# Kernel optimization log

Hardware: AMD Instinct MI355X
Metric: run time of the kernel (lower is better)

The kernel has to match this reference:

```python
import jax, jax.numpy as jnp
import numpy as np

B, S, D, H = 2, 2048, 512, 8
DK = D // H
MASK_VALUE = -1e9


def setup_inputs() -> dict:
    key = jax.random.key(0)
    ks = jax.random.split(key, 12)
    scale = 1.0 / np.sqrt(D)
    inp = {
        "query": jax.random.normal(ks[0], (B, S, D), jnp.float32),
        "key": jax.random.normal(ks[1], (B, S, D), jnp.float32),
        "value": jax.random.normal(ks[2], (B, S, D), jnp.float32),
        # causal mask, broadcastable over batch and heads
        "mask": jnp.tril(jnp.ones((S, S), jnp.int32))[None, None, :, :],
        "Wq": jax.random.normal(ks[3], (D, D), jnp.float32) * scale,
        "bq": jax.random.normal(ks[4], (D,), jnp.float32) * scale,
        "Wk": jax.random.normal(ks[5], (D, D), jnp.float32) * scale,
        "bk": jax.random.normal(ks[6], (D,), jnp.float32) * scale,
        "Wv": jax.random.normal(ks[7], (D, D), jnp.float32) * scale,
        "bv": jax.random.normal(ks[8], (D,), jnp.float32) * scale,
        "Wo": jax.random.normal(ks[9], (D, D), jnp.float32) * scale,
        "bo": jax.random.normal(ks[10], (D,), jnp.float32) * scale,
    }
    return inp


def reference(query, key, value, mask, Wq, bq, Wk, bk, Wv, bv, Wo, bo):
    # linear projections (torch Linear: x @ W.T + b)
    q = query @ Wq.T + bq
    k = key @ Wk.T + bk
    v = value @ Wv.T + bv
    # split heads: [B,S,D] -> [B,H,S,DK]
    q = q.reshape(B, S, H, DK).transpose(0, 2, 1, 3)
    k = k.reshape(B, S, H, DK).transpose(0, 2, 1, 3)
    v = v.reshape(B, S, H, DK).transpose(0, 2, 1, 3)
    # scaled dot-product attention with explicit [B,H,S,S] score matrix
    scores = jnp.einsum("bhqd,bhkd->bhqk", q, k) / jnp.sqrt(jnp.float32(DK))
    scores = jnp.where(mask == 0, jnp.float32(MASK_VALUE), scores)
    attn = jax.nn.softmax(scores, axis=-1)
    x = jnp.einsum("bhqk,bhkd->bhqd", attn, v)
    # merge heads: [B,H,S,DK] -> [B,S,D]
    x = x.transpose(0, 2, 1, 3).reshape(B, S, D)
    return x @ Wo.T + bo
```

## Files before the change

### kernel.cpp

```cpp
#include <hip/hip_runtime.h>
#include <hip/hip_bf16.h>

#define B_   2
#define S_   2048
#define D_   512
#define H_   8
#define DK_  64
#define M_   (B_*S_)

typedef float  floatx4 __attribute__((ext_vector_type(4)));
typedef __bf16 bf16x8  __attribute__((ext_vector_type(8)));

#define MFMA16x16x32(a,b,c) __builtin_amdgcn_mfma_f32_16x16x32_bf16((a),(b),(c),0,0,0)

#define PST 40
#define PBUF 2560

static __device__ __forceinline__ void load_lds16(const void* g, void* l) {
  __builtin_amdgcn_global_load_lds(
      (const __attribute__((address_space(1))) void*)g,
      (__attribute__((address_space(3))) void*)l,
      16, 0, 0);
}

static __device__ __forceinline__ bf16x8 cvt8(float4 a, float4 b) {
  bf16x8 r;
  r[0]=(__bf16)a.x; r[1]=(__bf16)a.y; r[2]=(__bf16)a.z; r[3]=(__bf16)a.w;
  r[4]=(__bf16)b.x; r[5]=(__bf16)b.y; r[6]=(__bf16)b.z; r[7]=(__bf16)b.w;
  return r;
}

static __device__ __forceinline__ int part_idx(int bh, int t, int s) {
  const int g = t >> 3;
  const int basec = (g == 2) ? 16 : ((g == 3) ? 40 : 0);
  return bh*72 + basec + (t - 8*g)*(g + 1) + s;
}


__global__ __launch_bounds__(256) void proj_qkv(
    const float* __restrict__ q_in, const float* __restrict__ k_in,
    const float* __restrict__ v_in,
    const float* __restrict__ Wq32, const float* __restrict__ Wk32,
    const float* __restrict__ Wv32,
    const float* __restrict__ bq, const float* __restrict__ bk,
    const float* __restrict__ bv,
    __bf16* __restrict__ Qb, __bf16* __restrict__ Kb, __bf16* __restrict__ Vtb)
{
  __shared__ __align__(16) __bf16 smem[4*PBUF];

  const int z = blockIdx.z;
  const float* X    = (z==0) ? q_in : (z==1) ? k_in : v_in;
  const float* W32  = (z==0) ? Wq32 : (z==1) ? Wk32 : Wv32;
  const float* bias = (z==0) ? bq : (z==1) ? bk : bv;

  const int m0 = blockIdx.x * 64;
  const int n0 = blockIdx.y * 64;
  const int tid  = threadIdx.x;
  const int w    = tid >> 6;
  const int lane = tid & 63;
  const int lcol = lane & 15;
  const int quad = lane >> 4;

  const int arow = tid >> 2, ac = (tid & 3) * 8;

  floatx4 zero = {0.f,0.f,0.f,0.f};
  floatx4 acc[4] = {zero, zero, zero, zero};

  float4 a0,a1,b0,b1;
  auto ldAB = [&](int k0) {
    const float* pa = X   + (size_t)(m0 + arow)*D_ + k0 + ac;
    const float* pb = W32 + (size_t)(n0 + arow)*D_ + k0 + ac;
    a0 = *(const float4*)pa; a1 = *(const float4*)(pa + 4);
    b0 = *(const float4*)pb; b1 = *(const float4*)(pb + 4);
  };
  auto wrAB = [&](int bsel) {
    *(bf16x8*)(smem + bsel*PBUF + arow*PST + ac)         = cvt8(a0, a1);
    *(bf16x8*)(smem + 2*PBUF + bsel*PBUF + arow*PST + ac) = cvt8(b0, b1);
  };

  ldAB(0); wrAB(0);
  for (int it = 0; it < 16; ++it) {
    __syncthreads();
    const bool havenext = (it + 1 < 16);
    if (havenext) ldAB((it+1)*32);
    const __bf16* ab = smem + (it&1)*PBUF;
    const __bf16* bb = smem + 2*PBUF + (it&1)*PBUF;
    const bf16x8 af = *(const bf16x8*)(ab + (w*16 + lcol)*PST + quad*8);
    bf16x8 bf[4];
#pragma unroll
    for (int nt = 0; nt < 4; ++nt)
      bf[nt] = *(const bf16x8*)(bb + (nt*16 + lcol)*PST + quad*8);
#pragma unroll
    for (int nt = 0; nt < 4; ++nt)
      acc[nt] = MFMA16x16x32(af, bf[nt], acc[nt]);
    if (havenext) wrAB((it+1)&1);
  }

  __syncthreads();
#pragma unroll
  for (int nt = 0; nt < 4; ++nt) {
    const int dk = nt*16 + lcol;
    const float bias_n = bias[n0 + dk];
#pragma unroll
    for (int r = 0; r < 4; ++r) {
      const int klo = w*16 + quad*4 + r;
      const float val = acc[nt][r] + bias_n;
      int off;
      if (z == 0) {
        off = klo*64 + dk;
      } else if (z == 1) {
        off = (((klo>>4)*2 + (dk>>5))*64 + ((dk>>3)&3)*16 + (klo&15))*8 + (dk&7);
      } else {
        off = (((dk>>4)*2 + (klo>>5))*64 + ((klo>>3)&3)*16 + (dk&15))*8 + (klo&7);
      }
      smem[off] = (__bf16)val;
    }
  }
  __syncthreads();

  __bf16* dst = (z==0) ? Qb : (z==1) ? Kb : Vtb;
  const int bb2 = m0 >> 11;
  const int hh  = n0 >> 6;
  const int cch = (m0 & 2047) >> 6;
  const size_t base = ((size_t)(bb2*H_ + hh))*(S_*DK_) + (size_t)cch*4096;
#pragma unroll
  for (int i = 0; i < 2; ++i) {
    const int u = i*256 + tid;
    *(bf16x8*)(dst + base + u*8) = *(const bf16x8*)(smem + u*8);
  }
}

__global__ __launch_bounds__(256) void attn_fwd(
    const __bf16* __restrict__ Qb, const __bf16* __restrict__ Kb,
    const __bf16* __restrict__ Vtb, __bf16* __restrict__ attnb,
    __bf16* __restrict__ Pb, float* __restrict__ Lb)
{
  __shared__ __align__(16) __bf16 kbuf[2][4096];
  __shared__ __align__(16) __bf16 vbuf[2][4096];
  __shared__ __align__(16) __bf16 pbuf[4][16*72];

  const int tid  = threadIdx.x;
  const int w    = tid >> 6;
  const int lane = tid & 63;
  const int lcol = lane & 15;
  const int quad = lane >> 4;
  const int hh = blockIdx.y;
  const int bb = blockIdx.z;

  const int wid = blockIdx.x;
  int t, s;
  if (wid < 8)       { t = wid;                  s = 0; }
  else if (wid < 24) { int u = wid - 8;  t = 8  + (u>>1); s = u & 1; }
  else if (wid < 48) { int u = wid - 24; int q3 = u/3; t = 16 + q3; s = u - 3*q3; }
  else               { int u = wid - 48; t = 24 + (u>>2); s = u & 3; }
  const bool single = (wid < 8);

  const int cbeg = s*8;
  const int cend = (cbeg + 8 < t + 1) ? (cbeg + 8) : (t + 1);
  const int q0  = t * 64;
  const int qr0 = q0 + w*16;

  const __bf16* Qp = Qb  + (size_t)(bb*H_ + hh) * S_ * DK_;
  const __bf16* Kp = Kb  + (size_t)(bb*H_ + hh) * S_ * DK_;
  const __bf16* Vp = Vtb + (size_t)(bb*H_ + hh) * DK_ * S_;

  const bf16x8 aq0 = *(const bf16x8*)(Qp + (size_t)(qr0 + lcol)*DK_ + quad*8);
  const bf16x8 aq1 = *(const bf16x8*)(Qp + (size_t)(qr0 + lcol)*DK_ + 32 + quad*8);

  floatx4 zero = {0.f,0.f,0.f,0.f};
  floatx4 acc[4] = {zero, zero, zero, zero};
  float lsum[4] = {0.f, 0.f, 0.f, 0.f};

  auto stage_chunk = [&](int bsel, int c) {
    const char* ksrc = (const char*)(Kp + (size_t)c * 4096);
    const char* vsrc = (const char*)(Vp + (size_t)c * 4096);
#pragma unroll
    for (int j = 0; j < 2; ++j) {
      const int off = w*2048 + j*1024;
      load_lds16(ksrc + off + lane*16, (char*)kbuf[bsel] + off);
      load_lds16(vsrc + off + lane*16, (char*)vbuf[bsel] + off);
    }
  };

  stage_chunk(0, cbeg);
  for (int c = cbeg; c < cend; ++c) {
    __syncthreads();
    if (c + 1 < cend) stage_chunk((c - cbeg + 1)&1, c+1);
    const int bsel = (c - cbeg) & 1;
    const int k0 = c * 64;
    const __bf16* kb = kbuf[bsel];
    const __bf16* vb = vbuf[bsel];

    floatx4 sc[4];
#pragma unroll
    for (int nt = 0; nt < 4; ++nt) {
      bf16x8 kf0 = *(const bf16x8*)(kb + (nt*2+0)*512 + lane*8);
      bf16x8 kf1 = *(const bf16x8*)(kb + (nt*2+1)*512 + lane*8);
      sc[nt] = MFMA16x16x32(aq1, kf1, MFMA16x16x32(aq0, kf0, zero));
    }

    const bool edge = (k0 + 63 > qr0);
#pragma unroll
    for (int nt = 0; nt < 4; ++nt) {
#pragma unroll
      for (int r = 0; r < 4; ++r) {
        float p = exp2f(sc[nt][r] * 0.18033688011112042f);
        if (edge) {
          const int qrow = qr0 + quad*4 + r;
          if (k0 + nt*16 + lcol > qrow) p = 0.f;
        }
        lsum[r] += p;
        pbuf[w][(quad*4 + r)*72 + nt*16 + lcol] = (__bf16)p;
      }
    }
    asm volatile("s_waitcnt lgkmcnt(0)" ::: "memory");

    const bf16x8 pa0 = *(const bf16x8*)(&pbuf[w][lcol*72 + quad*8]);
    const bf16x8 pa1 = *(const bf16x8*)(&pbuf[w][lcol*72 + 32 + quad*8]);
#pragma unroll
    for (int nt = 0; nt < 4; ++nt) {
      bf16x8 vf0 = *(const bf16x8*)(vb + (nt*2+0)*512 + lane*8);
      bf16x8 vf1 = *(const bf16x8*)(vb + (nt*2+1)*512 + lane*8);
      acc[nt] = MFMA16x16x32(pa0, vf0, acc[nt]);
      acc[nt] = MFMA16x16x32(pa1, vf1, acc[nt]);
    }
  }

  float tv[4];
#pragma unroll
  for (int r = 0; r < 4; ++r) {
    float v = lsum[r];
    v += __shfl_xor(v, 1, 16);
    v += __shfl_xor(v, 2, 16);
    v += __shfl_xor(v, 4, 16);
    v += __shfl_xor(v, 8, 16);
    tv[r] = v;
  }

  if (single) {
#pragma unroll
    for (int nt = 0; nt < 4; ++nt)
#pragma unroll
      for (int r = 0; r < 4; ++r) {
        const int q = qr0 + quad*4 + r;
        attnb[((size_t)(bb*S_ + q)) * D_ + hh*DK_ + nt*16 + lcol] =
            (__bf16)(acc[nt][r] / tv[r]);
      }
  } else {
    const int pidx = part_idx(bb*H_ + hh, t, s);
#pragma unroll
    for (int nt = 0; nt < 4; ++nt)
#pragma unroll
      for (int r = 0; r < 4; ++r)
        pbuf[w][(quad*4 + r)*72 + nt*16 + lcol] = (__bf16)acc[nt][r];
    asm volatile("s_waitcnt lgkmcnt(0)" ::: "memory");

    __bf16* pdst = Pb + (size_t)pidx*4096 + w*16*64;
#pragma unroll
    for (int i = 0; i < 2; ++i) {
      const int unit = i*64 + lane;
      const int row = unit >> 3, grp = unit & 7;
      *(bf16x8*)(pdst + row*64 + grp*8) =
          *(const bf16x8*)(&pbuf[w][row*72 + grp*8]);
    }
    if (lcol == 0) {
#pragma unroll
      for (int r = 0; r < 4; ++r)
        Lb[(size_t)pidx*64 + w*16 + quad*4 + r] = tv[r];
    }
  }
}

__global__ __launch_bounds__(512) void proj_out(
    const __bf16* __restrict__ attnb, const __bf16* __restrict__ Pb,
    const float* __restrict__ Lb, const float* __restrict__ Wo32,
    const float* __restrict__ bo, float* __restrict__ out)
{
  __shared__ __align__(16) __bf16 smem[8*PBUF];

  const int m0 = blockIdx.x * 64;
  const int n0 = blockIdx.y * 64;
  const int tid  = threadIdx.x;
  const int g    = tid >> 8;
  const int gt   = tid & 255;
  const int w    = tid >> 6;
  const int wg   = w & 3;
  const int lane = tid & 63;
  const int lcol = lane & 15;
  const int quad = lane >> 4;

  const int bb  = m0 >> 11;
  const int t   = (m0 & 2047) >> 6;
  const bool direct = (t < 8);
  const int nseg = (t >> 3) + 1;

  const int arow = gt >> 2, ac = (gt & 3) * 8;

  floatx4 zero = {0.f,0.f,0.f,0.f};
  floatx4 acc[4] = {zero, zero, zero, zero};

  bf16x8 av;
  bf16x8 pv[4]; float pl[4];
  float4 wb0, wb1;

  auto ldA = [&](int k0) {
    if (direct) {
      av = *(const bf16x8*)(attnb + (size_t)(m0 + arow)*D_ + k0 + ac);
    } else {
      const int hh = k0 >> 6;
      const int cblk = k0 & 63;
      const int pidx0 = part_idx(bb*H_ + hh, t, 0);
#pragma unroll 4
      for (int s2 = 0; s2 < 4; ++s2) {
        if (s2 < nseg) {
          pv[s2] = *(const bf16x8*)(Pb + (size_t)(pidx0 + s2)*4096
                                     + arow*64 + cblk + ac);
          pl[s2] = Lb[(size_t)(pidx0 + s2)*64 + arow];
        }
      }
    }
  };
  auto ldB = [&](int k0) {
    const float* pb = Wo32 + (size_t)(n0 + arow)*D_ + k0 + ac;
    wb0 = *(const float4*)pb; wb1 = *(const float4*)(pb + 4);
  };
  auto wrAB = [&](int bsel) {
    bf16x8 a;
    if (direct) {
      a = av;
    } else {
      float sum[8] = {0,0,0,0,0,0,0,0};
      float l = 0.f;
#pragma unroll 4
      for (int s2 = 0; s2 < 4; ++s2) {
        if (s2 < nseg) {
#pragma unroll
          for (int j = 0; j < 8; ++j) sum[j] += (float)pv[s2][j];
          l += pl[s2];
        }
      }
      const float rinv = 1.0f / l;
#pragma unroll
      for (int j = 0; j < 8; ++j) a[j] = (__bf16)(sum[j] * rinv);
    }
    *(bf16x8*)(smem + (g*2 + bsel)*PBUF + arow*PST + ac) = a;
    *(bf16x8*)(smem + 4*PBUF + (g*2 + bsel)*PBUF + arow*PST + ac)
        = cvt8(wb0, wb1);
  };

  const int kbase = g * 256;
  ldA(kbase); ldB(kbase); wrAB(0);
  for (int it = 0; it < 8; ++it) {
    __syncthreads();
    const bool havenext = (it + 1 < 8);
    if (havenext) { ldA(kbase + (it+1)*32); ldB(kbase + (it+1)*32); }
    const __bf16* ab = smem + (g*2 + (it&1))*PBUF;
    const __bf16* bbp = smem + 4*PBUF + (g*2 + (it&1))*PBUF;
    const bf16x8 af = *(const bf16x8*)(ab + (wg*16 + lcol)*PST + quad*8);
    bf16x8 bf[4];
#pragma unroll
    for (int nt = 0; nt < 4; ++nt)
      bf[nt] = *(const bf16x8*)(bbp + (nt*16 + lcol)*PST + quad*8);
#pragma unroll
    for (int nt = 0; nt < 4; ++nt)
      acc[nt] = MFMA16x16x32(af, bf[nt], acc[nt]);
    if (havenext) wrAB((it+1)&1);
  }

  __syncthreads();
  float* fbuf = (float*)smem;
  if (g == 1) {
#pragma unroll
    for (int nt = 0; nt < 4; ++nt)
#pragma unroll
      for (int r = 0; r < 4; ++r)
        fbuf[(wg*16 + quad*4 + r)*68 + nt*16 + lcol] = acc[nt][r];
  }
  __syncthreads();
  if (g == 0) {
#pragma unroll
    for (int nt = 0; nt < 4; ++nt) {
      const int n = n0 + nt*16 + lcol;
      const float bias_n = bo[n];
#pragma unroll
      for (int r = 0; r < 4; ++r) {
        const int row = wg*16 + quad*4 + r;
        const float val = acc[nt][r] + fbuf[row*68 + nt*16 + lcol] + bias_n;
        out[(size_t)(m0 + row) * D_ + n] = val;
      }
    }
  }
}

extern "C" void kernel_launch(void* const* d_in, const int* in_sizes, int n_in,
                              void* d_out, int out_size, void* d_ws, size_t ws_size,
                              hipStream_t stream) {
  const float* q_in = (const float*)d_in[0];
  const float* k_in = (const float*)d_in[1];
  const float* v_in = (const float*)d_in[2];
  const float* Wq = (const float*)d_in[4];
  const float* bq = (const float*)d_in[5];
  const float* Wk = (const float*)d_in[6];
  const float* bk = (const float*)d_in[7];
  const float* Wv = (const float*)d_in[8];
  const float* bv = (const float*)d_in[9];
  const float* Wo = (const float*)d_in[10];
  const float* bo = (const float*)d_in[11];
  float* out = (float*)d_out;

  __bf16* ws    = (__bf16*)d_ws;
  __bf16* Qb    = ws;
  __bf16* Kb    = ws + 1*2097152;
  __bf16* Vtb   = ws + 2*2097152;
  __bf16* attnb = ws + 3*2097152;
  __bf16* Pb    = ws + 4*2097152;
  float*  Lb    = (float*)(Pb + 1152*4096);

  proj_qkv<<<dim3(M_/64, D_/64, 3), dim3(256), 0, stream>>>(
      q_in, k_in, v_in, Wq, Wk, Wv, bq, bk, bv, Qb, Kb, Vtb);

  attn_fwd<<<dim3(80, H_, B_), dim3(256), 0, stream>>>(
      Qb, Kb, Vtb, attnb, Pb, Lb);

  proj_out<<<dim3(M_/64, D_/64), dim3(512), 0, stream>>>(
      attnb, Pb, Lb, Wo, bo, out);
}
```

Baseline: 162.7 us.

## Split attention KV into 4-chunk segments and split-K the QKV projection

The attention kernel now splits each query tile's causal key range into segments of 4 chunks instead of 8, raising the grid from 80 to 144 blocks per head and shortening the longest block. The output projection merges up to 8 partials, using a new partial index layout and a larger workspace. The QKV projection uses 512 threads, with two thread groups each doing half of K, then reduces the two halves through LDS. This aims to fix load imbalance and low occupancy, at the cost of more partial-result traffic and extra reduction work.

```diff
diff --git a/kernel.cpp b/kernel.cpp
--- a/kernel.cpp
+++ b/kernel.cpp
@@ -30,14 +30,13 @@
   return r;
 }
 
-static __device__ __forceinline__ int part_idx(int bh, int t, int s) {
-  const int g = t >> 3;
-  const int basec = (g == 2) ? 16 : ((g == 3) ? 40 : 0);
-  return bh*72 + basec + (t - 8*g)*(g + 1) + s;
-}
-
-
-__global__ __launch_bounds__(256) void proj_qkv(
+static __device__ __forceinline__ int part_idx4(int bh, int t, int s) {
+  const int k = t >> 2;
+  return bh*140 + (2*k*(k+1) - 4) + (t - 4*k)*(k + 1) + s;
+}
+
+
+__global__ __launch_bounds__(512) void proj_qkv(
     const float* __restrict__ q_in, const float* __restrict__ k_in,
     const float* __restrict__ v_in,
     const float* __restrict__ Wq32, const float* __restrict__ Wk32,
@@ -46,7 +45,7 @@
     const float* __restrict__ bv,
     __bf16* __restrict__ Qb, __bf16* __restrict__ Kb, __bf16* __restrict__ Vtb)
 {
-  __shared__ __align__(16) __bf16 smem[4*PBUF];
+  __shared__ __align__(16) __bf16 smem[8*PBUF];
 
   const int z = blockIdx.z;
   const float* X    = (z==0) ? q_in : (z==1) ? k_in : v_in;
@@ -56,12 +55,14 @@
   const int m0 = blockIdx.x * 64;
   const int n0 = blockIdx.y * 64;
   const int tid  = threadIdx.x;
-  const int w    = tid >> 6;
+  const int g    = tid >> 8;
+  const int gt   = tid & 255;
+  const int wg   = (tid >> 6) & 3;
   const int lane = tid & 63;
   const int lcol = lane & 15;
   const int quad = lane >> 4;
 
-  const int arow = tid >> 2, ac = (tid & 3) * 8;
+  const int arow = gt >> 2, ac = (gt & 3) * 8;
 
   floatx4 zero = {0.f,0.f,0.f,0.f};
   floatx4 acc[4] = {zero, zero, zero, zero};
@@ -74,18 +75,19 @@
     b0 = *(const float4*)pb; b1 = *(const float4*)(pb + 4);
   };
   auto wrAB = [&](int bsel) {
-    *(bf16x8*)(smem + bsel*PBUF + arow*PST + ac)         = cvt8(a0, a1);
-    *(bf16x8*)(smem + 2*PBUF + bsel*PBUF + arow*PST + ac) = cvt8(b0, b1);
-  };
-
-  ldAB(0); wrAB(0);
-  for (int it = 0; it < 16; ++it) {
+    *(bf16x8*)(smem + (g*2 + bsel)*PBUF + arow*PST + ac)          = cvt8(a0, a1);
+    *(bf16x8*)(smem + 4*PBUF + (g*2 + bsel)*PBUF + arow*PST + ac) = cvt8(b0, b1);
+  };
+
+  const int kbase = g * 256;
+  ldAB(kbase); wrAB(0);
+  for (int it = 0; it < 8; ++it) {
     __syncthreads();
-    const bool havenext = (it + 1 < 16);
-    if (havenext) ldAB((it+1)*32);
-    const __bf16* ab = smem + (it&1)*PBUF;
-    const __bf16* bb = smem + 2*PBUF + (it&1)*PBUF;
-    const bf16x8 af = *(const bf16x8*)(ab + (w*16 + lcol)*PST + quad*8);
+    const bool havenext = (it + 1 < 8);
+    if (havenext) ldAB(kbase + (it+1)*32);
+    const __bf16* ab = smem + (g*2 + (it&1))*PBUF;
+    const __bf16* bb = smem + 4*PBUF + (g*2 + (it&1))*PBUF;
+    const bf16x8 af = *(const bf16x8*)(ab + (wg*16 + lcol)*PST + quad*8);
     bf16x8 bf[4];
 #pragma unroll
     for (int nt = 0; nt < 4; ++nt)
@@ -97,23 +99,35 @@
   }
 
   __syncthreads();
-#pragma unroll
-  for (int nt = 0; nt < 4; ++nt) {
-    const int dk = nt*16 + lcol;
-    const float bias_n = bias[n0 + dk];
-#pragma unroll
-    for (int r = 0; r < 4; ++r) {
-      const int klo = w*16 + quad*4 + r;
-      const float val = acc[nt][r] + bias_n;
-      int off;
-      if (z == 0) {
-        off = klo*64 + dk;
-      } else if (z == 1) {
-        off = (((klo>>4)*2 + (dk>>5))*64 + ((dk>>3)&3)*16 + (klo&15))*8 + (dk&7);
-      } else {
-        off = (((dk>>4)*2 + (klo>>5))*64 + ((klo>>3)&3)*16 + (dk&15))*8 + (klo&7);
-      }
-      smem[off] = (__bf16)val;
+  float* fbuf = (float*)smem;
+  __bf16* sbuf = smem + 8704;
+  if (g == 1) {
+#pragma unroll
+    for (int nt = 0; nt < 4; ++nt)
+#pragma unroll
+      for (int r = 0; r < 4; ++r)
+        fbuf[(wg*16 + quad*4 + r)*68 + nt*16 + lcol] = acc[nt][r];
+  }
+  __syncthreads();
+  if (g == 0) {
+#pragma unroll
+    for (int nt = 0; nt < 4; ++nt) {
+      const int dk = nt*16 + lcol;
+      const float bias_n = bias[n0 + dk];
+#pragma unroll
+      for (int r = 0; r < 4; ++r) {
+        const int klo = wg*16 + quad*4 + r;
+        const float val = acc[nt][r] + fbuf[klo*68 + dk] + bias_n;
+        int off;
+        if (z == 0) {
+          off = klo*64 + dk;
+        } else if (z == 1) {
+          off = (((klo>>4)*2 + (dk>>5))*64 + ((dk>>3)&3)*16 + (klo&15))*8 + (dk&7);
+        } else {
+          off = (((dk>>4)*2 + (klo>>5))*64 + ((klo>>3)&3)*16 + (dk&15))*8 + (klo&7);
+        }
+        sbuf[off] = (__bf16)val;
+      }
     }
   }
   __syncthreads();
@@ -123,11 +137,7 @@
   const int hh  = n0 >> 6;
   const int cch = (m0 & 2047) >> 6;
   const size_t base = ((size_t)(bb2*H_ + hh))*(S_*DK_) + (size_t)cch*4096;
-#pragma unroll
-  for (int i = 0; i < 2; ++i) {
-    const int u = i*256 + tid;
-    *(bf16x8*)(dst + base + u*8) = *(const bf16x8*)(smem + u*8);
-  }
+  *(bf16x8*)(dst + base + tid*8) = *(const bf16x8*)(sbuf + tid*8);
 }
 
 __global__ __launch_bounds__(256) void attn_fwd(
@@ -148,15 +158,17 @@
   const int bb = blockIdx.z;
 
   const int wid = blockIdx.x;
-  int t, s;
-  if (wid < 8)       { t = wid;                  s = 0; }
-  else if (wid < 24) { int u = wid - 8;  t = 8  + (u>>1); s = u & 1; }
-  else if (wid < 48) { int u = wid - 24; int q3 = u/3; t = 16 + q3; s = u - 3*q3; }
-  else               { int u = wid - 48; t = 24 + (u>>2); s = u & 3; }
-  const bool single = (wid < 8);
-
-  const int cbeg = s*8;
-  const int cend = (cbeg + 8 < t + 1) ? (cbeg + 8) : (t + 1);
+  int k = 0;
+#pragma unroll
+  for (int j = 1; j < 8; ++j)
+    if (wid >= 2*j*(j+1)) k = j;
+  const int u = wid - 2*k*(k+1);
+  const int t = 4*k + u/(k+1);
+  const int s = u - (u/(k+1))*(k+1);
+  const bool single = (k == 0);
+
+  const int cbeg = s*4;
+  const int cend = (cbeg + 4 < t + 1) ? (cbeg + 4) : (t + 1);
   const int q0  = t * 64;
   const int qr0 = q0 + w*16;
 
@@ -247,7 +259,7 @@
             (__bf16)(acc[nt][r] / tv[r]);
       }
   } else {
-    const int pidx = part_idx(bb*H_ + hh, t, s);
+    const int pidx = part_idx4(bb*H_ + hh, t, s);
 #pragma unroll
     for (int nt = 0; nt < 4; ++nt)
 #pragma unroll
@@ -283,16 +295,15 @@
   const int tid  = threadIdx.x;
   const int g    = tid >> 8;
   const int gt   = tid & 255;
-  const int w    = tid >> 6;
-  const int wg   = w & 3;
+  const int wg   = (tid >> 6) & 3;
   const int lane = tid & 63;
   const int lcol = lane & 15;
   const int quad = lane >> 4;
 
   const int bb  = m0 >> 11;
   const int t   = (m0 & 2047) >> 6;
-  const bool direct = (t < 8);
-  const int nseg = (t >> 3) + 1;
+  const bool direct = (t < 4);
+  const int nseg = (t >> 2) + 1;
 
   const int arow = gt >> 2, ac = (gt & 3) * 8;
 
@@ -300,7 +311,7 @@
   floatx4 acc[4] = {zero, zero, zero, zero};
 
   bf16x8 av;
-  bf16x8 pv[4]; float pl[4];
+  bf16x8 pv[8]; float pl[8];
   float4 wb0, wb1;
 
   auto ldA = [&](int k0) {
@@ -309,9 +320,9 @@
     } else {
       const int hh = k0 >> 6;
       const int cblk = k0 & 63;
-      const int pidx0 = part_idx(bb*H_ + hh, t, 0);
-#pragma unroll 4
-      for (int s2 = 0; s2 < 4; ++s2) {
+      const int pidx0 = part_idx4(bb*H_ + hh, t, 0);
+#pragma unroll 8
+      for (int s2 = 0; s2 < 8; ++s2) {
         if (s2 < nseg) {
           pv[s2] = *(const bf16x8*)(Pb + (size_t)(pidx0 + s2)*4096
                                      + arow*64 + cblk + ac);
@@ -331,8 +342,8 @@
     } else {
       float sum[8] = {0,0,0,0,0,0,0,0};
       float l = 0.f;
-#pragma unroll 4
-      for (int s2 = 0; s2 < 4; ++s2) {
+#pragma unroll 8
+      for (int s2 = 0; s2 < 8; ++s2) {
         if (s2 < nseg) {
 #pragma unroll
           for (int j = 0; j < 8; ++j) sum[j] += (float)pv[s2][j];
@@ -414,12 +425,12 @@
   __bf16* Vtb   = ws + 2*2097152;
   __bf16* attnb = ws + 3*2097152;
   __bf16* Pb    = ws + 4*2097152;
-  float*  Lb    = (float*)(Pb + 1152*4096);
-
-  proj_qkv<<<dim3(M_/64, D_/64, 3), dim3(256), 0, stream>>>(
+  float*  Lb    = (float*)(Pb + 2240*4096);
+
+  proj_qkv<<<dim3(M_/64, D_/64, 3), dim3(512), 0, stream>>>(
       q_in, k_in, v_in, Wq, Wk, Wv, bq, bk, bv, Qb, Kb, Vtb);
 
-  attn_fwd<<<dim3(80, H_, B_), dim3(256), 0, stream>>>(
+  attn_fwd<<<dim3(144, H_, B_), dim3(256), 0, stream>>>(
       Qb, Kb, Vtb, attnb, Pb, Lb);
 
   proj_out<<<dim3(M_/64, D_/64), dim3(512), 0, stream>>>(
```

Result: slower. 173.2 us (+6.5%).
